# Optimization experiments

Measured on AMD Instinct MI355X. Metric: run time of the kernel, lower is better.

The kernel has to match this reference:

```python
import jax, jax.numpy as jnp
import numpy as np

N = 50_000          # num nodes
E = 800_000         # num edges
D = 32              # input/hidden dim
NUM_LAYERS = 6
BOUNDARY_FILL = 100.0


def setup_inputs() -> dict:
    key = jax.random.key(0)
    ks = jax.random.split(key, 10)
    return {
        "node_in": jax.random.randint(ks[0], (E,), 0, N, dtype=jnp.int32),
        "node_out": jax.random.randint(ks[1], (E,), 0, N, dtype=jnp.int32),
        "edge_weight": jax.random.uniform(ks[2], (E,), dtype=jnp.float32),
        "h_index": 0,
        "query_weight": jax.random.normal(ks[3], (1, D), dtype=jnp.float32) * 0.1,
        "rel_W": jax.random.normal(ks[4], (NUM_LAYERS, D, D), dtype=jnp.float32) / np.sqrt(D),
        "rel_b": jnp.zeros((NUM_LAYERS, D), dtype=jnp.float32),
        "lin_W": jax.random.normal(ks[5], (NUM_LAYERS, 13 * D, D), dtype=jnp.float32) / np.sqrt(13 * D),
        "lin_b": jnp.zeros((NUM_LAYERS, D), dtype=jnp.float32),
        "mlp_W1": jax.random.normal(ks[6], (2 * D, 2 * D), dtype=jnp.float32) / np.sqrt(2 * D),
        "mlp_b1": jnp.zeros((2 * D,), dtype=jnp.float32),
        "mlp_W2": jax.random.normal(ks[7], (2 * D, 1), dtype=jnp.float32) / np.sqrt(2 * D),
        "mlp_b2": jnp.zeros((1,), dtype=jnp.float32),
    }


def reference(node_in, node_out, edge_weight, h_index, query_weight,
              rel_W, rel_b, lin_W, lin_b, mlp_W1, mlp_b1, mlp_W2, mlp_b2):
    # query = self.query(r_index) with r_index = 0, batch = 1
    query = query_weight[:1]                                # [1, D]
    boundary = jnp.full((N, 1, D), BOUNDARY_FILL, dtype=jnp.float32)
    boundary = boundary.at[h_index, 0].set(0.0)             # boundary[h][0] = 0

    loop = jnp.arange(N, dtype=node_out.dtype)
    node_in_aug = jnp.concatenate([node_in, loop])          # boundary rows act as self-loop msgs
    node_out_aug = jnp.concatenate([node_out, loop])
    ew_aug = jnp.concatenate([edge_weight, jnp.ones((N,), edge_weight.dtype)])

    degree_out = jax.ops.segment_sum(edge_weight, node_out, num_segments=N) + 1.0  # [N]
    count = jax.ops.segment_sum(jnp.ones_like(ew_aug), node_out_aug, num_segments=N)  # [N]

    # PNA degree scalers (identity / amplification / attenuation)
    scale = jnp.log(degree_out)
    scale = scale / jnp.mean(scale)
    scales = jnp.stack([jnp.ones_like(scale), scale, 1.0 / jnp.clip(scale, 1e-2)], axis=-1)  # [N,3]

    w = ew_aug[:, None, None]
    cnt = count[:, None, None]

    layer_input = boundary
    predecessor = jnp.zeros((N,), dtype=node_in.dtype)
    for i in range(NUM_LAYERS):
        # dependent relation embedding: relation_linear(query), relation id 0 everywhere
        rel_input = query @ rel_W[i] + rel_b[i]             # [1, D]
        message = layer_input[node_in] * rel_input[None]    # [E,1,D] distmult
        msg_aug = jnp.concatenate([message, boundary], axis=0)  # [E+N,1,D]
        wm = msg_aug * w

        mean = jax.ops.segment_sum(wm, node_out_aug, num_segments=N) / cnt
        sq_mean = jax.ops.segment_sum(jnp.square(msg_aug) * w, node_out_aug, num_segments=N) / cnt
        mx = jax.ops.segment_max(wm, node_out_aug, num_segments=N)
        mn = jax.ops.segment_min(wm, node_out_aug, num_segments=N)
        std = jnp.sqrt(jnp.clip(sq_mean - jnp.square(mean), 1e-6))

        feats = jnp.stack([mean, mx, mn, std], axis=-1).reshape(N, 1, 4 * D)
        update = (feats[..., None] * scales[:, None, None, :]).reshape(N, 1, 12 * D)
        hidden = jax.nn.relu(
            jnp.concatenate([layer_input, update], axis=-1) @ lin_W[i] + lin_b[i]
        )  # [N,1,D]

        if i == NUM_LAYERS - 1:
            # predecessor: source node of the strongest incoming (weighted) message
            msg_score = wm.sum(axis=(1, 2))                 # [E+N]
            seg_max = jax.ops.segment_max(msg_score, node_out_aug, num_segments=N)
            cand = jnp.where(msg_score >= seg_max[node_out_aug], node_in_aug,
                             jnp.asarray(N, node_in_aug.dtype))
            predecessor = jax.ops.segment_min(cand, node_out_aug, num_segments=N)
        layer_input = hidden

    node_query = jnp.broadcast_to(query[None], (N, 1, D))
    output = jnp.concatenate([layer_input, node_query], axis=-1)  # [N,1,2D]
    feature = jnp.transpose(output, (1, 0, 2))                    # [1,N,2D]
    h = jax.nn.relu(feature @ mlp_W1 + mlp_b1)
    score = (h @ mlp_W2 + mlp_b2).squeeze(-1)                     # [1,N]
    return score, predecessor
```

## Files before the change

kernel.cpp:

```cpp
#include <hip/hip_runtime.h>
#include <math.h>

#define NN 50000
#define EE 800000
#define DD 32
#define BSTR 64
#define NPART 8
#define CPB 128

typedef float v2f __attribute__((ext_vector_type(2)));

__device__ inline v2f vmax2(v2f a, v2f b){ v2f r; r[0]=fmaxf(a[0],b[0]); r[1]=fmaxf(a[1],b[1]); return r; }
__device__ inline v2f vmin2(v2f a, v2f b){ v2f r; r[0]=fminf(a[0],b[0]); r[1]=fminf(a[1],b[1]); return r; }


__global__ __launch_bounds__(256) void k_zero(float* p, int count){
  int i = blockIdx.x*256 + threadIdx.x;
  if (i < count) p[i] = 0.f;
}

__global__ __launch_bounds__(256) void k_fillcsr(const int* __restrict__ node_in,
                                                 const int* __restrict__ node_out,
                                                 const float* __restrict__ ew,
                                                 int* __restrict__ cursor,
                                                 int2* __restrict__ csr){
  int part  = blockIdx.x & (NPART-1);
  int group = blockIdx.x >> 3;
  const int per = (EE + CPB - 1) / CPB;
  int e0 = group * per;
  int e1 = (e0 + per < EE) ? (e0 + per) : EE;
  unsigned lo = (unsigned)part * 6250u;
  unsigned hi = lo + 6250u;
  for (int e = e0 + threadIdx.x; e < e1; e += 256){
    unsigned o = (unsigned)node_out[e];
    if (o >= lo && o < hi){
      int pos = atomicAdd(&cursor[o], 1);
      int2 v; v.x = node_in[e]; v.y = __float_as_int(ew[e]);
      csr[o*BSTR + pos] = v;
    }
  }
}

__global__ __launch_bounds__(256) void k_sumw(int2* __restrict__ csr,
                                              const int* __restrict__ cursor,
                                              float* __restrict__ deg_w,
                                              float* __restrict__ logsum){
  __shared__ float sf[256];
  int t = threadIdx.x;
  int g = t >> 3, lane = t & 7;
  int n = blockIdx.x*32 + g;
  float s = 0.f;
  if (n < NN){
    int deg = cursor[n];
    int2* row = csr + n*BSTR;
    for (int i = lane; i < deg; i += 8) s += __int_as_float(row[i].y);
    s += __shfl_xor(s, 1);
    s += __shfl_xor(s, 2);
    s += __shfl_xor(s, 4);
    row[deg + lane] = make_int2(0, 0);
    if (lane == 0) deg_w[n] = s;
  }
  sf[t] = (n < NN && lane == 0) ? logf(s + 1.f) : 0.f;
  __syncthreads();
  for (int off = 128; off > 0; off >>= 1){
    if (t < off) sf[t] += sf[t+off];
    __syncthreads();
  }
  if (t == 0) atomicAdd(logsum, sf[0]);
}

__global__ __launch_bounds__(448) void k_prep2(const float* __restrict__ qw,
                                               const float* __restrict__ rel_W,
                                               const float* __restrict__ rel_b,
                                               const float* __restrict__ W1,
                                               const float* __restrict__ b1,
                                               const float* __restrict__ lin_W,
                                               float* __restrict__ rel6,
                                               float* __restrict__ qc,
                                               float* __restrict__ wcol,
                                               float* __restrict__ Wt){
  if (blockIdx.x < 48){
    int lw = blockIdx.x;
    int l = lw >> 3, w = lw & 7;
    int k = threadIdx.x;
    if (k >= 416) return;
    int row;
    if (k < 32) row = k;
    else {
      int kk = k - 32;
      int kp = kk / 3, s = kk - kp*3;
      row = 32 + (kp >> 2)*12 + (kp & 3)*3 + s;
    }
    float4 v = *(const float4*)(lin_W + (size_t)l*13312 + row*32 + w*4);
    ((float4*)Wt)[(size_t)lw*416 + k] = v;
  } else {
    int t = threadIdx.x;
    if (t < 192){
      int l = t >> 5, j = t & 31;
      float s = rel_b[t];
      for (int d = 0; d < 32; ++d) s += qw[d] * rel_W[l*1024 + d*32 + j];
      rel6[t] = s;
    } else if (t < 256){
      int j = t - 192;
      float s = b1[j];
      for (int k = 0; k < 32; ++k) s += qw[k] * W1[(32+k)*64 + j];
      qc[j] = s;
    } else if (t < 288){
      int j = t - 256;
      float s = 0.f;
      for (int k = 0; k < 32; ++k) s += lin_W[k*32 + j];
      wcol[j] = s;
    }
  }
}

__global__ __launch_bounds__(512, 6) void k_layer0(const float* __restrict__ rel6,
                                               const int* __restrict__ cursor,
                                               const int2* __restrict__ csr,
                                               const int* __restrict__ hidx,
                                               const float* __restrict__ Wt,
                                               const float* __restrict__ lin_b,
                                               const float* __restrict__ wcol,
                                               const float* __restrict__ deg_w,
                                               const float* __restrict__ logsum,
                                               float* __restrict__ h_next){
  __shared__ float sh[128*65];
  int tid = threadIdx.x;
  int base = blockIdx.x * 64;
  int hv0 = *hidx;

  {
    int nl   = tid >> 3;
    int quad = tid & 7;
    float4 r4 = ((const float4*)(rel6))[quad];
    int n0 = base + nl;
    int n = (n0 < NN) ? n0 : NN-1;
    int deg = cursor[n];
    int s0 = n*BSTR, s1 = s0 + deg;
    float S1=0.f, S2=0.f, M=-INFINITY, m=INFINITY;

#define ACCS(C) { \
    float w  = __int_as_float(C.y); \
    float hv = (C.x == hv0) ? 0.f : 100.f; \
    float wm = w * hv; \
    S1 += wm; S2 += wm * hv; \
    M = fmaxf(M, wm); m = fminf(m, wm); }

    int2 cA = csr[s0],   cB = csr[s0+1], cC = csr[s0+2], cD = csr[s0+3];
    int e = s0;
    for (; e + 4 <= s1; e += 4){
      int2 nA = csr[e+4], nB = csr[e+5], nC = csr[e+6], nD = csr[e+7];
      ACCS(cA) ACCS(cB) ACCS(cC) ACCS(cD)
      cA = nA; cB = nB; cC = nC; cD = nD;
    }
    if (e < s1){
      ACCS(cA)
      if (e + 1 < s1){
        ACCS(cB)
        if (e + 2 < s1) ACCS(cC)
      }
    }
#undef ACCS

    float bnd = (n == hv0) ? 0.f : 100.f;
    float cntf = (float)(deg + 1);
#define FIN(cc, rc) { \
    float mxv, mnv; \
    if (deg > 0){ \
      float em = (rc >= 0.f) ? rc*M : rc*m; \
      float en = (rc >= 0.f) ? rc*m : rc*M; \
      mxv = fmaxf(em, bnd); mnv = fminf(en, bnd); \
    } else { mxv = bnd; mnv = bnd; } \
    float meanv = (rc*S1 + bnd) / cntf; \
    float sq    = (rc*rc*S2 + bnd*bnd) / cntf; \
    float sdv   = sqrtf(fmaxf(sq - meanv*meanv, 1e-6f)); \
    int d = quad*4 + cc; \
    sh[(d*4+0)*65 + nl] = meanv; \
    sh[(d*4+1)*65 + nl] = mxv; \
    sh[(d*4+2)*65 + nl] = mnv; \
    sh[(d*4+3)*65 + nl] = sdv; }
    FIN(0, r4.x) FIN(1, r4.y) FIN(2, r4.z) FIN(3, r4.w)
#undef FIN
  }
  __syncthreads();

  {
    int lane = tid & 63;
    int grp = __builtin_amdgcn_readfirstlane(tid >> 6);
    int j0 = grp * 4;
    const float* Ww = Wt + (size_t)grp*1664 + 128;
    int n0 = base + lane;
    int n = (n0 < NN) ? n0 : NN-1;
    float mean = *logsum / (float)NN;
    float sc = logf(deg_w[n] + 1.f) / mean;
    float iv = 1.f / fmaxf(sc, 0.01f);
    float bndn = (n == hv0) ? 0.f : 100.f;
    v2f a01p={0,0}, a23p={0,0}, a01s={0,0}, a23s={0,0}, a01i={0,0}, a23i={0,0};

    for (int kp = 0; kp < 128; ++kp){
      float f = sh[kp*65 + lane];
      const v2f* wp = (const v2f*)(Ww + kp*12);
      v2f fv; fv[0]=f; fv[1]=f;
      a01p += fv*wp[0];  a23p += fv*wp[1];
      a01s += fv*wp[2];  a23s += fv*wp[3];
      a01i += fv*wp[4];  a23i += fv*wp[5];
    }
    v2f sc2; sc2[0]=sc; sc2[1]=sc;
    v2f iv2; iv2[0]=iv; iv2[1]=iv;
    v2f a01 = a01p + sc2*a01s + iv2*a01i;
    v2f a23 = a23p + sc2*a23s + iv2*a23i;
    a01[0] += lin_b[j0+0] + bndn*wcol[j0+0];
    a01[1] += lin_b[j0+1] + bndn*wcol[j0+1];
    a23[0] += lin_b[j0+2] + bndn*wcol[j0+2];
    a23[1] += lin_b[j0+3] + bndn*wcol[j0+3];

    if (n0 < NN){
      float vs[4] = { a01[0], a01[1], a23[0], a23[1] };
      #pragma unroll
      for (int j = 0; j < 4; ++j)
        h_next[n0*32 + j0 + j] = fmaxf(vs[j], 0.f);
    }
  }
}

template<int MODE>
__global__ __launch_bounds__(512, 6) void k_layer(const float* __restrict__ h,
                                               const float* __restrict__ rel6,
                                               const int* __restrict__ cursor,
                                               const int2* __restrict__ csr,
                                               const int* __restrict__ hidx,
                                               const float* __restrict__ tdot,
                                               const float* __restrict__ Wt,
                                               const float* __restrict__ lin_b,
                                               const float* __restrict__ deg_w,
                                               const float* __restrict__ logsum,
                                               float* __restrict__ h_next,
                                               float* __restrict__ pred_out,
                                               const float* __restrict__ qc,
                                               const float* __restrict__ W1,
                                               const float* __restrict__ W2,
                                               const float* __restrict__ b2,
                                               float* __restrict__ out_score,
                                               float* __restrict__ tdot_out,
                                               int l){
  __shared__ float sh[128*65];
  int tid = threadIdx.x;
  int base = blockIdx.x * 64;
  int hv0 = *hidx;

  {
    int nl   = tid >> 3;
    int quad = tid & 7;
    float4 r4 = ((const float4*)(rel6 + l*32))[quad];
    int n0 = base + nl;
    bool valid = n0 < NN;
    int n = valid ? n0 : NN-1;
    int deg = cursor[n];
    int s0 = n*BSTR, s1 = s0 + deg;
    v2f S1xy={0,0}, S1zw={0,0}, S2xy={0,0}, S2zw={0,0};
    v2f Mxy={-INFINITY,-INFINITY}, Mzw={-INFINITY,-INFINITY};
    v2f mxy={ INFINITY, INFINITY}, mzw={ INFINITY, INFINITY};
    float best=-INFINITY; int bi=NN;

#define ACC1(C, A, T) { \
    float w = __int_as_float(C.y); \
    v2f wv; wv[0]=w; wv[1]=w; \
    v2f axy; axy[0]=A.x; axy[1]=A.y; \
    v2f azw; azw[0]=A.z; azw[1]=A.w; \
    v2f pxy = wv*axy, pzw = wv*azw; \
    S1xy += pxy; S1zw += pzw; \
    S2xy += pxy*axy; S2zw += pzw*azw; \
    Mxy = vmax2(Mxy, pxy); Mzw = vmax2(Mzw, pzw); \
    mxy = vmin2(mxy, pxy); mzw = vmin2(mzw, pzw); \
    if (MODE==2){ \
      float sv = w*T; \
      if (sv > best){ best = sv; bi = C.x; } \
      else if (sv == best && C.x < bi) bi = C.x; \
    } }

    int2 cA = csr[s0],   cB = csr[s0+1], cC = csr[s0+2], cD = csr[s0+3];
    int e = s0;
    for (; e + 4 <= s1; e += 4){
      float4 a  = ((const float4*)(h + cA.x*32))[quad];
      float4 b  = ((const float4*)(h + cB.x*32))[quad];
      float4 c4 = ((const float4*)(h + cC.x*32))[quad];
      float4 d4 = ((const float4*)(h + cD.x*32))[quad];
      float tA=0.f, tB=0.f, tC=0.f, tD=0.f;
      if (MODE==2){ tA = tdot[cA.x]; tB = tdot[cB.x]; tC = tdot[cC.x]; tD = tdot[cD.x]; }
      int2 nA = csr[e+4], nB = csr[e+5], nC = csr[e+6], nD = csr[e+7];
      ACC1(cA, a, tA)
      ACC1(cB, b, tB)
      ACC1(cC, c4, tC)
      ACC1(cD, d4, tD)
      cA = nA; cB = nB; cC = nC; cD = nD;
    }
    if (e < s1){
      float4 a = ((const float4*)(h + cA.x*32))[quad];
      float tA = 0.f; if (MODE==2) tA = tdot[cA.x];
      ACC1(cA, a, tA)
      if (e + 1 < s1){
        float4 b = ((const float4*)(h + cB.x*32))[quad];
        float tB = 0.f; if (MODE==2) tB = tdot[cB.x];
        ACC1(cB, b, tB)
        if (e + 2 < s1){
          float4 c4 = ((const float4*)(h + cC.x*32))[quad];
          float tC = 0.f; if (MODE==2) tC = tdot[cC.x];
          ACC1(cC, c4, tC)
        }
      }
    }
#undef ACC1

    float bnd = (n == hv0) ? 0.f : 100.f;
    float cntf = (float)(deg + 1);
#define FIN(cc, rc, S1c, S2c, Mc, mc) { \
    float mxv, mnv; \
    if (deg > 0){ \
      float em = (rc >= 0.f) ? rc*Mc : rc*mc; \
      float en = (rc >= 0.f) ? rc*mc : rc*Mc; \
      mxv = fmaxf(em, bnd); mnv = fminf(en, bnd); \
    } else { mxv = bnd; mnv = bnd; } \
    float meanv = (rc*S1c + bnd) / cntf; \
    float sq    = (rc*rc*S2c + bnd*bnd) / cntf; \
    float sdv   = sqrtf(fmaxf(sq - meanv*meanv, 1e-6f)); \
    int d = quad*4 + cc; \
    sh[(d*4+0)*65 + nl] = meanv; \
    sh[(d*4+1)*65 + nl] = mxv; \
    sh[(d*4+2)*65 + nl] = mnv; \
    sh[(d*4+3)*65 + nl] = sdv; }
    FIN(0, r4.x, S1xy[0], S2xy[0], Mxy[0], mxy[0])
    FIN(1, r4.y, S1xy[1], S2xy[1], Mxy[1], mxy[1])
    FIN(2, r4.z, S1zw[0], S2zw[0], Mzw[0], mzw[0])
    FIN(3, r4.w, S1zw[1], S2zw[1], Mzw[1], mzw[1])
#undef FIN
    if (MODE==2 && valid && quad == 0){
      float ss = (n == hv0) ? 0.f : 3200.f;
      if (ss > best){ best = ss; bi = n; }
      else if (ss == best && n < bi) bi = n;
      pred_out[n] = (float)bi;
    }
  }
  __syncthreads();

  {
    int lane = tid & 63;
    int grp = __builtin_amdgcn_readfirstlane(tid >> 6);
    int j0 = grp * 4;
    const float* Ww = Wt + (size_t)(l*8 + grp)*1664;
    int n0 = base + lane;
    int n = (n0 < NN) ? n0 : NN-1;
    float mean = *logsum / (float)NN;
    float sc = logf(deg_w[n] + 1.f) / mean;
    float iv = 1.f / fmaxf(sc, 0.01f);
    const float4* hr = (const float4*)(h + (size_t)n*32);
    float4 x0=hr[0],x1=hr[1],x2=hr[2],x3=hr[3],x4=hr[4],x5=hr[5],x6=hr[6],x7=hr[7];
    v2f a01p={0,0}, a23p={0,0}, a01s={0,0}, a23s={0,0}, a01i={0,0}, a23i={0,0};

#define KONE(XV, K) { \
    v2f xv2; xv2[0] = XV; xv2[1] = XV; \
    const v2f* wr2 = (const v2f*)(Ww + (K)*4); \
    a01p += xv2 * wr2[0]; \
    a23p += xv2 * wr2[1]; }
#define KQ(X, KB) KONE(X.x, KB+0) KONE(X.y, KB+1) KONE(X.z, KB+2) KONE(X.w, KB+3)
    KQ(x0, 0) KQ(x1, 4) KQ(x2, 8) KQ(x3, 12)
    KQ(x4, 16) KQ(x5, 20) KQ(x6, 24) KQ(x7, 28)
#undef KQ
#undef KONE

    const float* Wf = Ww + 128;
    for (int kp = 0; kp < 128; ++kp){
      float f = sh[kp*65 + lane];
      const v2f* wp = (const v2f*)(Wf + kp*12);
      v2f fv; fv[0]=f; fv[1]=f;
      a01p += fv*wp[0];  a23p += fv*wp[1];
      a01s += fv*wp[2];  a23s += fv*wp[3];
      a01i += fv*wp[4];  a23i += fv*wp[5];
    }
    v2f sc2; sc2[0]=sc; sc2[1]=sc;
    v2f iv2; iv2[0]=iv; iv2[1]=iv;
    v2f a01 = a01p + sc2*a01s + iv2*a01i;
    v2f a23 = a23p + sc2*a23s + iv2*a23i;
    a01[0] += lin_b[l*32 + j0 + 0];
    a01[1] += lin_b[l*32 + j0 + 1];
    a23[0] += lin_b[l*32 + j0 + 2];
    a23[1] += lin_b[l*32 + j0 + 3];

    float v0r = fmaxf(a01[0], 0.f), v1r = fmaxf(a01[1], 0.f);
    float v2r = fmaxf(a23[0], 0.f), v3r = fmaxf(a23[1], 0.f);

    if (MODE==0 || MODE==1){
      if (n0 < NN){
        h_next[n0*32 + j0 + 0] = v0r;
        h_next[n0*32 + j0 + 1] = v1r;
        h_next[n0*32 + j0 + 2] = v2r;
        h_next[n0*32 + j0 + 3] = v3r;
      }
    }
    if (MODE==1){
      __syncthreads();
      sh[(j0+0)*65 + lane] = v0r;
      sh[(j0+1)*65 + lane] = v1r;
      sh[(j0+2)*65 + lane] = v2r;
      sh[(j0+3)*65 + lane] = v3r;
      __syncthreads();
      if (tid < 64){
        const float* relr = rel6 + 5*32;
        float s = 0.f;
        #pragma unroll
        for (int d = 0; d < 32; ++d) s += sh[d*65 + tid] * relr[d];
        if (base + tid < NN) tdot_out[base + tid] = s;
      }
    } else if (MODE==2){
      __syncthreads();
      sh[(j0+0)*65 + lane] = v0r;
      sh[(j0+1)*65 + lane] = v1r;
      sh[(j0+2)*65 + lane] = v2r;
      sh[(j0+3)*65 + lane] = v3r;
      __syncthreads();
      int node = tid & 63;
      int grp2 = __builtin_amdgcn_readfirstlane(tid >> 6);
      int jm = grp2*8;
      v2f b0, b1v, b2v, b3;
      b0[0]=qc[jm+0]; b0[1]=qc[jm+1]; b1v[0]=qc[jm+2]; b1v[1]=qc[jm+3];
      b2v[0]=qc[jm+4]; b2v[1]=qc[jm+5]; b3[0]=qc[jm+6]; b3[1]=qc[jm+7];
      for (int k = 0; k < 32; ++k){
        float xv = sh[k*65 + node];
        const v2f* wr = (const v2f*)(W1 + k*64 + jm);
        v2f xv2; xv2[0]=xv; xv2[1]=xv;
        b0 += xv2*wr[0]; b1v += xv2*wr[1]; b2v += xv2*wr[2]; b3 += xv2*wr[3];
      }
      float part = fmaxf(b0[0],0.f)*W2[jm+0] + fmaxf(b0[1],0.f)*W2[jm+1]
                 + fmaxf(b1v[0],0.f)*W2[jm+2] + fmaxf(b1v[1],0.f)*W2[jm+3]
                 + fmaxf(b2v[0],0.f)*W2[jm+4] + fmaxf(b2v[1],0.f)*W2[jm+5]
                 + fmaxf(b3[0],0.f)*W2[jm+6] + fmaxf(b3[1],0.f)*W2[jm+7];
      sh[2080 + node*9 + grp2] = part;
      __syncthreads();
      if (tid < 64){
        float s = b2[0];
        #pragma unroll
        for (int g = 0; g < 8; ++g) s += sh[2080 + tid*9 + g];
        if (base + tid < NN) out_score[base + tid] = s;
      }
    }
  }
}

extern "C" void kernel_launch(void* const* d_in, const int* in_sizes, int n_in,
                              void* d_out, int out_size, void* d_ws, size_t ws_size,
                              hipStream_t stream){
  const int*   node_in  = (const int*)d_in[0];
  const int*   node_out = (const int*)d_in[1];
  const float* ew       = (const float*)d_in[2];
  const int*   hidx     = (const int*)d_in[3];
  const float* qw       = (const float*)d_in[4];
  const float* rel_W    = (const float*)d_in[5];
  const float* rel_b    = (const float*)d_in[6];
  const float* lin_W    = (const float*)d_in[7];
  const float* lin_b    = (const float*)d_in[8];
  const float* W1       = (const float*)d_in[9];
  const float* b1       = (const float*)d_in[10];
  const float* W2       = (const float*)d_in[11];
  const float* b2       = (const float*)d_in[12];
  float* out_score = (float*)d_out;
  float* out_pred  = out_score + NN;

  char* w = (char*)d_ws;
  size_t off = 0;
  auto take = [&](size_t bytes)->char*{
    char* p = w + off;
    off = (off + bytes + 255) & ~(size_t)255;
    return p;
  };
  size_t bucket_elems = (size_t)NN * BSTR;
  int2*  csr      = (int2*)take(bucket_elems*8);
  char*  zb       = take((size_t)NN*4 + (size_t)NN*4 + 256);
  int*   cursor   = (int*)zb;
  float* deg_w    = (float*)(cursor + NN);
  float* logsum   = (float*)(deg_w + NN);
  int zc = NN + NN + 64;

  float* rel6      = (float*)take(192*4);
  float* qc        = (float*)take(64*4);
  float* wcol      = (float*)take(32*4);
  float* Wt        = (float*)take((size_t)48*416*16);
  float* tdot      = (float*)take((size_t)NN*4);
  float* h_a       = (float*)take((size_t)NN*32*4);
  float* h_b       = (float*)take((size_t)NN*32*4);

  int nsb = (NN + 31) / 32;
  int nlb = (NN + 63) / 64;
  k_zero   <<<(zc+255)/256, 256, 0, stream>>>((float*)zb, zc);
  k_fillcsr<<<NPART*CPB, 256, 0, stream>>>(node_in, node_out, ew, cursor, csr);
  k_sumw   <<<nsb, 256, 0, stream>>>(csr, cursor, deg_w, logsum);
  k_prep2  <<<49, 448, 0, stream>>>(qw, rel_W, rel_b, W1, b1, lin_W,
                                    rel6, qc, wcol, Wt);

  k_layer0<<<nlb, 512, 0, stream>>>(rel6, cursor, csr, hidx, Wt, lin_b,
                                    wcol, deg_w, logsum, h_a);

  float* hc = h_a;
  float* hn = h_b;
  for (int l = 1; l < 6; ++l){
    if (l == 5){
      k_layer<2><<<nlb, 512, 0, stream>>>(hc, rel6, cursor, csr, hidx, tdot,
                                          Wt, lin_b, deg_w, logsum,
                                          hn, out_pred,
                                          qc, W1, W2, b2, out_score, tdot, l);
    } else if (l == 4){
      k_layer<1><<<nlb, 512, 0, stream>>>(hc, rel6, cursor, csr, hidx, tdot,
                                          Wt, lin_b, deg_w, logsum,
                                          hn, out_pred,
                                          qc, W1, W2, b2, out_score, tdot, l);
    } else {
      k_layer<0><<<nlb, 512, 0, stream>>>(hc, rel6, cursor, csr, hidx, tdot,
                                          Wt, lin_b, deg_w, logsum,
                                          hn, out_pred,
                                          qc, W1, W2, b2, out_score, tdot, l);
    }
    float* t1 = hc; hc = hn; hn = t1;
  }
}
```

Before: 378.0 us.

## Process nodes in degree-sorted order to balance per-wavefront edge loops

Adds a histogram, scan and scatter pass that builds a permutation of nodes sorted by in-degree, descending. The layer kernels then process nodes through this permutation, so threads in a wavefront walk similar-length edge lists, and outputs are scattered back to the original node indices. The goal is to cut divergence and tail imbalance in the per-node aggregation loops. The cost is three extra small kernel launches, an indirection load per node, and scattered non-coalesced writes of hidden rows and outputs.

```diff
diff --git a/kernel.cpp b/kernel.cpp
--- a/kernel.cpp
+++ b/kernel.cpp
@@ -38,6 +38,39 @@
       int2 v; v.x = node_in[e]; v.y = __float_as_int(ew[e]);
       csr[o*BSTR + pos] = v;
     }
+  }
+}
+
+__global__ __launch_bounds__(256) void k_hist(const int* __restrict__ cursor,
+                                              int* __restrict__ bins){
+  __shared__ int lh[64];
+  int t = threadIdx.x;
+  if (t < 64) lh[t] = 0;
+  __syncthreads();
+  int n = blockIdx.x*256 + t;
+  if (n < NN){
+    int d = cursor[n]; if (d > 63) d = 63;
+    atomicAdd(&lh[d], 1);
+  }
+  __syncthreads();
+  if (t < 64 && lh[t]) atomicAdd(&bins[t], lh[t]);
+}
+
+__global__ void k_scan(const int* __restrict__ bins, int* __restrict__ binoff){
+  if (threadIdx.x == 0){
+    int acc = 0;
+    for (int d = 63; d >= 0; --d){ binoff[d] = acc; acc += bins[d]; }
+  }
+}
+
+__global__ __launch_bounds__(256) void k_scatter(const int* __restrict__ cursor,
+                                                 int* __restrict__ binoff,
+                                                 int* __restrict__ perm){
+  int n = blockIdx.x*256 + threadIdx.x;
+  if (n < NN){
+    int d = cursor[n]; if (d > 63) d = 63;
+    int pos = atomicAdd(&binoff[d], 1);
+    perm[pos] = n;
   }
 }
 
@@ -123,6 +156,7 @@
                                                const float* __restrict__ wcol,
                                                const float* __restrict__ deg_w,
                                                const float* __restrict__ logsum,
+                                               const int* __restrict__ perm,
                                                float* __restrict__ h_next){
   __shared__ float sh[128*65];
   int tid = threadIdx.x;
@@ -134,7 +168,7 @@
     int quad = tid & 7;
     float4 r4 = ((const float4*)(rel6))[quad];
     int n0 = base + nl;
-    int n = (n0 < NN) ? n0 : NN-1;
+    int n = perm[(n0 < NN) ? n0 : NN-1];
     int deg = cursor[n];
     int s0 = n*BSTR, s1 = s0 + deg;
     float S1=0.f, S2=0.f, M=-INFINITY, m=INFINITY;
@@ -190,7 +224,7 @@
     int j0 = grp * 4;
     const float* Ww = Wt + (size_t)grp*1664 + 128;
     int n0 = base + lane;
-    int n = (n0 < NN) ? n0 : NN-1;
+    int n = perm[(n0 < NN) ? n0 : NN-1];
     float mean = *logsum / (float)NN;
     float sc = logf(deg_w[n] + 1.f) / mean;
     float iv = 1.f / fmaxf(sc, 0.01f);
@@ -218,7 +252,7 @@
       float vs[4] = { a01[0], a01[1], a23[0], a23[1] };
       #pragma unroll
       for (int j = 0; j < 4; ++j)
-        h_next[n0*32 + j0 + j] = fmaxf(vs[j], 0.f);
+        h_next[n*32 + j0 + j] = fmaxf(vs[j], 0.f);
     }
   }
 }
@@ -234,6 +268,7 @@
                                                const float* __restrict__ lin_b,
                                                const float* __restrict__ deg_w,
                                                const float* __restrict__ logsum,
+                                               const int* __restrict__ perm,
                                                float* __restrict__ h_next,
                                                float* __restrict__ pred_out,
                                                const float* __restrict__ qc,
@@ -254,7 +289,7 @@
     float4 r4 = ((const float4*)(rel6 + l*32))[quad];
     int n0 = base + nl;
     bool valid = n0 < NN;
-    int n = valid ? n0 : NN-1;
+    int n = perm[valid ? n0 : NN-1];
     int deg = cursor[n];
     int s0 = n*BSTR, s1 = s0 + deg;
     v2f S1xy={0,0}, S1zw={0,0}, S2xy={0,0}, S2zw={0,0};
@@ -348,7 +383,7 @@
     int j0 = grp * 4;
     const float* Ww = Wt + (size_t)(l*8 + grp)*1664;
     int n0 = base + lane;
-    int n = (n0 < NN) ? n0 : NN-1;
+    int n = perm[(n0 < NN) ? n0 : NN-1];
     float mean = *logsum / (float)NN;
     float sc = logf(deg_w[n] + 1.f) / mean;
     float iv = 1.f / fmaxf(sc, 0.01f);
@@ -390,10 +425,10 @@
 
     if (MODE==0 || MODE==1){
       if (n0 < NN){
-        h_next[n0*32 + j0 + 0] = v0r;
-        h_next[n0*32 + j0 + 1] = v1r;
-        h_next[n0*32 + j0 + 2] = v2r;
-        h_next[n0*32 + j0 + 3] = v3r;
+        h_next[n*32 + j0 + 0] = v0r;
+        h_next[n*32 + j0 + 1] = v1r;
+        h_next[n*32 + j0 + 2] = v2r;
+        h_next[n*32 + j0 + 3] = v3r;
       }
     }
     if (MODE==1){
@@ -408,7 +443,7 @@
         float s = 0.f;
         #pragma unroll
         for (int d = 0; d < 32; ++d) s += sh[d*65 + tid] * relr[d];
-        if (base + tid < NN) tdot_out[base + tid] = s;
+        if (base + tid < NN) tdot_out[perm[base + tid]] = s;
       }
     } else if (MODE==2){
       __syncthreads();
@@ -439,7 +474,7 @@
         float s = b2[0];
         #pragma unroll
         for (int g = 0; g < 8; ++g) s += sh[2080 + tid*9 + g];
-        if (base + tid < NN) out_score[base + tid] = s;
+        if (base + tid < NN) out_score[perm[base + tid]] = s;
       }
     }
   }
@@ -473,47 +508,54 @@
   };
   size_t bucket_elems = (size_t)NN * BSTR;
   int2*  csr      = (int2*)take(bucket_elems*8);
-  char*  zb       = take((size_t)NN*4 + (size_t)NN*4 + 256);
+  char*  zb       = take((size_t)NN*4 + (size_t)NN*4 + 512);
   int*   cursor   = (int*)zb;
   float* deg_w    = (float*)(cursor + NN);
   float* logsum   = (float*)(deg_w + NN);
-  int zc = NN + NN + 64;
+  int*   bins     = (int*)(logsum + 64);
+  int zc = NN + NN + 64 + 64;
 
   float* rel6      = (float*)take(192*4);
   float* qc        = (float*)take(64*4);
   float* wcol      = (float*)take(32*4);
   float* Wt        = (float*)take((size_t)48*416*16);
+  int*   binoff    = (int*)take(64*4);
+  int*   perm      = (int*)take((size_t)NN*4);
   float* tdot      = (float*)take((size_t)NN*4);
   float* h_a       = (float*)take((size_t)NN*32*4);
   float* h_b       = (float*)take((size_t)NN*32*4);
 
+  int nb  = (NN + 255) / 256;
   int nsb = (NN + 31) / 32;
   int nlb = (NN + 63) / 64;
   k_zero   <<<(zc+255)/256, 256, 0, stream>>>((float*)zb, zc);
   k_fillcsr<<<NPART*CPB, 256, 0, stream>>>(node_in, node_out, ew, cursor, csr);
+  k_hist   <<<nb, 256, 0, stream>>>(cursor, bins);
+  k_scan   <<<1, 64, 0, stream>>>(bins, binoff);
+  k_scatter<<<nb, 256, 0, stream>>>(cursor, binoff, perm);
   k_sumw   <<<nsb, 256, 0, stream>>>(csr, cursor, deg_w, logsum);
   k_prep2  <<<49, 448, 0, stream>>>(qw, rel_W, rel_b, W1, b1, lin_W,
                                     rel6, qc, wcol, Wt);
 
   k_layer0<<<nlb, 512, 0, stream>>>(rel6, cursor, csr, hidx, Wt, lin_b,
-                                    wcol, deg_w, logsum, h_a);
+                                    wcol, deg_w, logsum, perm, h_a);
 
   float* hc = h_a;
   float* hn = h_b;
   for (int l = 1; l < 6; ++l){
     if (l == 5){
       k_layer<2><<<nlb, 512, 0, stream>>>(hc, rel6, cursor, csr, hidx, tdot,
-                                          Wt, lin_b, deg_w, logsum,
+                                          Wt, lin_b, deg_w, logsum, perm,
                                           hn, out_pred,
                                           qc, W1, W2, b2, out_score, tdot, l);
     } else if (l == 4){
       k_layer<1><<<nlb, 512, 0, stream>>>(hc, rel6, cursor, csr, hidx, tdot,
-                                          Wt, lin_b, deg_w, logsum,
+                                          Wt, lin_b, deg_w, logsum, perm,
                                           hn, out_pred,
                                           qc, W1, W2, b2, out_score, tdot, l);
     } else {
       k_layer<0><<<nlb, 512, 0, stream>>>(hc, rel6, cursor, csr, hidx, tdot,
-                                          Wt, lin_b, deg_w, logsum,
+                                          Wt, lin_b, deg_w, logsum, perm,
                                           hn, out_pred,
                                           qc, W1, W2, b2, out_score, tdot, l);
     }
```

New measurement: 510.7 us. 1.35x slower.
